# Kernel optimization log

Measured on AMD Instinct MI355X. Metric: run time of the kernel, lower is better.

Reference implementation:

```python
import jax, jax.numpy as jnp
import numpy as np

R = 16
LORA_ALPHA = 32
SCALING = LORA_ALPHA / R  # use_rslora=False -> alpha/r = 2.0


def fwht(x):
    """Normalized fast Walsh-Hadamard transform along last axis (power-of-2 dim)."""
    n = x.shape[-1]
    batch = x.shape[:-1]
    h = 1
    while h < n:  # static loop, log2(n) iterations
        x = x.reshape(*batch, n // (2 * h), 2, h)
        a = x[..., 0, :]
        b = x[..., 1, :]
        x = jnp.stack([a + b, a - b], axis=-2).reshape(*batch, n)
        h *= 2
    return x * np.float32(1.0 / np.sqrt(n))


def quant_int8_ste(x):
    """Simulated symmetric per-row int8 quantization with straight-through estimator."""
    s = jnp.max(jnp.abs(x), axis=-1, keepdims=True) * np.float32(1.0 / 127.0)
    s = jnp.maximum(s, np.float32(1e-8))
    q = jnp.clip(jnp.round(x / s), -127.0, 127.0) * s
    return x + jax.lax.stop_gradient(q - x)


def setup_inputs() -> dict:
    key = jax.random.key(0)
    k1, k2, k3, k4 = jax.random.split(key, 4)
    B, S, D_in, D_out = 4, 2048, 4096, 4096
    x = jax.random.normal(k1, (B, S, D_in), dtype=jnp.float32)
    weight = jax.random.normal(k2, (D_out, D_in), dtype=jnp.float32) * np.float32(0.02)
    lora_A = jax.random.normal(k3, (R, D_in), dtype=jnp.float32) * np.float32(0.02)
    lora_B = jax.random.normal(k4, (D_out, R), dtype=jnp.float32) * np.float32(0.02)
    return {"x": x, "weight": weight, "lora_A": lora_A, "lora_B": lora_B}


def reference(x, weight, lora_A, lora_B):
    B, S, D_in = x.shape
    x2 = x.reshape(-1, D_in)  # [B*S, D_in]
    # Hadamard-rotate + quantize both operands (rotation is orthogonal, so
    # (xH)(WH)^T == xW^T up to quantization error) then GEMM.
    xq = quant_int8_ste(fwht(x2))          # [B*S, D_in]
    wq = quant_int8_ste(fwht(weight))      # [D_out, D_in]
    out = xq @ wq.T                        # [B*S, D_out]
    # LoRA side path (dropout p=0): B(A x) * scaling
    lora = (x2 @ lora_A.T) @ lora_B.T * np.float32(SCALING)
    return (out + lora).reshape(B, S, -1)
```

## Files before the change

### kernel.cpp

```cpp
#include <hip/hip_runtime.h>
#include <stdint.h>

typedef int v4i __attribute__((ext_vector_type(4)));

#define GLD_LDS16(gp, lp)                                                              \
  __builtin_amdgcn_global_load_lds((const __attribute__((address_space(1))) void*)(gp), \
                                   (__attribute__((address_space(3))) void*)(lp), 16, 0, 0)

__device__ __forceinline__ v4i lds_read_b128(uint32_t off) {
  v4i r;
  asm volatile("ds_read_b128 %0, %1" : "=v"(r) : "v"(off));
  return r;
}

#define LGKM_FENCE()                                   \
  do {                                                 \
    asm volatile("s_waitcnt lgkmcnt(0)" ::: "memory"); \
    __builtin_amdgcn_sched_barrier(0);                 \
  } while (0)

__device__ __forceinline__ void fwht16(float v[16]) {
#pragma unroll
  for (int h = 1; h < 16; h <<= 1) {
#pragma unroll
    for (int i = 0; i < 16; ++i) {
      if (!(i & h)) {
        float a = v[i], b = v[i | h];
        v[i] = a + b;
        v[i | h] = a - b;
      }
    }
  }
}

__global__ __launch_bounds__(256) void fwht_quant_kernel(const float* __restrict__ X,
                                                         int8_t* __restrict__ Q,
                                                         float* __restrict__ S) {
  const int row = blockIdx.x;
  const int t = threadIdx.x;
  __shared__ float lds[4224];
  __shared__ float wred[4];

  const float* xr = X + (size_t)row * 4096;
  float v[16];
  {
    const float4* p = reinterpret_cast<const float4*>(xr) + t * 4;
    float4 a = p[0], b = p[1], c = p[2], d = p[3];
    v[0] = a.x; v[1] = a.y; v[2] = a.z; v[3] = a.w;
    v[4] = b.x; v[5] = b.y; v[6] = b.z; v[7] = b.w;
    v[8] = c.x; v[9] = c.y; v[10] = c.z; v[11] = c.w;
    v[12] = d.x; v[13] = d.y; v[14] = d.z; v[15] = d.w;
  }
  fwht16(v);
#pragma unroll
  for (int e = 0; e < 16; ++e) {
    int idx = t * 16 + e;
    lds[idx + (idx >> 5)] = v[e];
  }
  __syncthreads();
#pragma unroll
  for (int e = 0; e < 16; ++e) {
    int idx = ((t >> 4) << 8) + (e << 4) + (t & 15);
    v[e] = lds[idx + (idx >> 5)];
  }
  fwht16(v);
#pragma unroll
  for (int e = 0; e < 16; ++e) {
    int idx = ((t >> 4) << 8) + (e << 4) + (t & 15);
    lds[idx + (idx >> 5)] = v[e];
  }
  __syncthreads();
#pragma unroll
  for (int e = 0; e < 16; ++e) {
    int idx = (e << 8) + t;
    v[e] = lds[idx + (idx >> 5)];
  }
  fwht16(v);

  float m = 0.f;
#pragma unroll
  for (int e = 0; e < 16; ++e) {
    v[e] *= 0.015625f;
    m = fmaxf(m, fabsf(v[e]));
  }
#pragma unroll
  for (int off = 32; off > 0; off >>= 1) m = fmaxf(m, __shfl_xor(m, off));
  if ((t & 63) == 0) wred[t >> 6] = m;
  __syncthreads();
  m = fmaxf(fmaxf(wred[0], wred[1]), fmaxf(wred[2], wred[3]));
  const float s = fmaxf(m * (1.0f / 127.0f), 1e-8f);
  if (t == 0) S[row] = s;
  int8_t* qr = Q + (size_t)row * 4096;
#pragma unroll
  for (int e = 0; e < 16; ++e) {
    float q = rintf(v[e] / s);
    q = fminf(fmaxf(q, -127.f), 127.f);
    qr[(e << 8) + t] = (int8_t)(int)q;
  }
}

__global__ __launch_bounds__(256) void lora_t_partial_kernel(const float* __restrict__ X,
                                                             const float* __restrict__ A,
                                                             float* __restrict__ tpart) {
  __shared__ float As[16][512];
  const int t = threadIdx.x;
  const int kc = blockIdx.y;
  const int row = blockIdx.x * 256 + t;
  for (int i = t; i < 2048; i += 256) {
    int r = i >> 7;
    int c4 = i & 127;
    reinterpret_cast<float4*>(&As[r][0])[c4] =
        reinterpret_cast<const float4*>(A + (size_t)r * 4096 + kc * 512)[c4];
  }
  __syncthreads();
  float acc[16];
#pragma unroll
  for (int r = 0; r < 16; ++r) acc[r] = 0.f;
  const float* xr = X + (size_t)row * 4096 + kc * 512;
  for (int k = 0; k < 512; k += 4) {
    float4 xv = *reinterpret_cast<const float4*>(xr + k);
#pragma unroll
    for (int r = 0; r < 16; ++r) {
      float4 av = *reinterpret_cast<const float4*>(&As[r][k]);
      acc[r] += xv.x * av.x + xv.y * av.y + xv.z * av.z + xv.w * av.w;
    }
  }
  float* tp = tpart + ((size_t)kc * 8192 + row) * 16;
#pragma unroll
  for (int r = 0; r < 16; ++r) tp[r] = acc[r];
}

__global__ __launch_bounds__(256) void lora_t_reduce_kernel(const float* __restrict__ tpart,
                                                            float* __restrict__ tmat) {
  int i = blockIdx.x * 256 + threadIdx.x;
  float s = 0.f;
#pragma unroll
  for (int kc = 0; kc < 8; ++kc) s += tpart[(size_t)kc * 131072 + i];
  tmat[i] = s;
}

__global__ __launch_bounds__(512, 2) void gemm_i8_kernel(
    const int8_t* __restrict__ Aq, const int8_t* __restrict__ Bq,
    const float* __restrict__ Sx, const float* __restrict__ Sw,
    const float* __restrict__ Tm, const float* __restrict__ LB,
    float* __restrict__ out) {
  __shared__ __align__(16) char smem[131072];

  const int tid = threadIdx.x;
  const int lane = tid & 63;
  const int w = tid >> 6;
  const int wm = w >> 2;
  const int wn = w & 3;

  int bid = (int)blockIdx.x;
  bid = (bid & 7) * 64 + (bid >> 3);
  const int bm = bid >> 4;
  const int bn = bid & 15;

  const int8_t* Ag = Aq + (size_t)bm * 256 * 4096;
  const int8_t* Bg = Bq + (size_t)bn * 256 * 4096;

  const uint32_t sbase = (uint32_t)(uintptr_t)(void*)smem;

  const int L0 = w * 1024 + lane * 16;
  const int rS0 = L0 >> 6;
  const int rS1 = rS0 + 128;
  const int cS0 = (((lane & 3) ^ ((rS0 >> 1) & 3)) << 4);

#define STAGE(gbase, ldsOff, kByte)                                                      \
  do {                                                                                   \
    GLD_LDS16((gbase) + (size_t)rS0 * 4096 + (kByte) + cS0, smem + (ldsOff) + w * 1024); \
    GLD_LDS16((gbase) + (size_t)rS1 * 4096 + (kByte) + cS0,                              \
              smem + (ldsOff) + 8192 + w * 1024);                                        \
  } while (0)

  int aoff[8], boff[4];
  const int cc = lane >> 4;
#pragma unroll
  for (int mi = 0; mi < 8; ++mi) {
    int r = wm * 128 + mi * 16 + (lane & 15);
    aoff[mi] = r * 64 + ((cc ^ ((r >> 1) & 3)) << 4);
  }
#pragma unroll
  for (int ni = 0; ni < 4; ++ni) {
    int r = wn * 64 + ni * 16 + (lane & 15);
    boff[ni] = r * 64 + ((cc ^ ((r >> 1) & 3)) << 4);
  }

  v4i acc[8][4];
#pragma unroll
  for (int i = 0; i < 8; ++i)
#pragma unroll
    for (int n = 0; n < 4; ++n) {
      v4i z = {0, 0, 0, 0};
      acc[i][n] = z;
    }

  STAGE(Ag, 0, 0);
  STAGE(Bg, 32768, 0);
  STAGE(Ag, 16384, 64);
  STAGE(Bg, 49152, 64);
  asm volatile("s_waitcnt vmcnt(4)" ::: "memory");
  __builtin_amdgcn_s_barrier();
  __builtin_amdgcn_sched_barrier(0);

#define MFMA_CLUSTER(MH)                                                                  \
  do {                                                                                    \
    __builtin_amdgcn_s_setprio(1);                                                        \
    _Pragma("unroll") for (int i = 0; i < 4; ++i) _Pragma("unroll") for (int n = 0;       \
                                                                        n < 4; ++n)       \
        acc[(MH)*4 + i][n] =                                                              \
        __builtin_amdgcn_mfma_i32_16x16x64_i8(af[i], bf[n], acc[(MH)*4 + i][n], 0, 0, 0); \
    __builtin_amdgcn_s_setprio(0);                                                        \
  } while (0)

#pragma unroll 1
  for (int t = 0; t < 32; ++t) {
    const uint32_t Ab = sbase + (t & 1) * 65536;
    const uint32_t Bb = Ab + 32768;
    const int nx = ((t & 1) ^ 1) * 65536;
    const bool pf = (t + 1) < 32;
    const int kB = (t + 1) << 7;
    v4i af[4], bf[4];

    if (pf) STAGE(Ag, nx + 0, kB);
#pragma unroll
    for (int i = 0; i < 4; ++i) af[i] = lds_read_b128(Ab + aoff[i]);
#pragma unroll
    for (int n = 0; n < 4; ++n) bf[n] = lds_read_b128(Bb + boff[n]);
    __builtin_amdgcn_s_barrier();
    LGKM_FENCE();
    MFMA_CLUSTER(0);
    __builtin_amdgcn_s_barrier();

    if (pf) STAGE(Bg, nx + 32768, kB);
#pragma unroll
    for (int i = 0; i < 4; ++i) af[i] = lds_read_b128(Ab + aoff[4 + i]);
    __builtin_amdgcn_s_barrier();
    LGKM_FENCE();
    MFMA_CLUSTER(1);
    if (pf)
      asm volatile("s_waitcnt vmcnt(4)" ::: "memory");
    else
      asm volatile("s_waitcnt vmcnt(0)" ::: "memory");
    __builtin_amdgcn_s_barrier();
    __builtin_amdgcn_sched_barrier(0);

    if (pf) STAGE(Ag, nx + 16384, kB + 64);
#pragma unroll
    for (int i = 0; i < 4; ++i) af[i] = lds_read_b128(Ab + 16384 + aoff[i]);
#pragma unroll
    for (int n = 0; n < 4; ++n) bf[n] = lds_read_b128(Bb + 16384 + boff[n]);
    __builtin_amdgcn_s_barrier();
    LGKM_FENCE();
    MFMA_CLUSTER(0);
    __builtin_amdgcn_s_barrier();

    if (pf) STAGE(Bg, nx + 49152, kB + 64);
#pragma unroll
    for (int i = 0; i < 4; ++i) af[i] = lds_read_b128(Ab + 16384 + aoff[4 + i]);
    __builtin_amdgcn_s_barrier();
    LGKM_FENCE();
    MFMA_CLUSTER(1);
    if (pf) asm volatile("s_waitcnt vmcnt(4)" ::: "memory");
    __builtin_amdgcn_s_barrier();
    __builtin_amdgcn_sched_barrier(0);
  }

  __syncthreads();
  float* tl = (float*)smem;
  float* bl = (float*)(smem + 17408);
  for (int i = tid; i < 1024; i += 512) {
    int r = i >> 2, q4 = (i & 3) * 4;
    float4 tv = *reinterpret_cast<const float4*>(Tm + (size_t)(bm * 256 + r) * 16 + q4);
    tl[r * 17 + q4 + 0] = tv.x;
    tl[r * 17 + q4 + 1] = tv.y;
    tl[r * 17 + q4 + 2] = tv.z;
    tl[r * 17 + q4 + 3] = tv.w;
    float4 bv = *reinterpret_cast<const float4*>(LB + (size_t)(bn * 256 + r) * 16 + q4);
    bl[r * 17 + q4 + 0] = bv.x;
    bl[r * 17 + q4 + 1] = bv.y;
    bl[r * 17 + q4 + 2] = bv.z;
    bl[r * 17 + q4 + 3] = bv.w;
  }
  __syncthreads();

  float blv[4][16], swv[4];
#pragma unroll
  for (int ni = 0; ni < 4; ++ni) {
    int cl = wn * 64 + ni * 16 + (lane & 15);
    swv[ni] = Sw[bn * 256 + cl];
#pragma unroll
    for (int q = 0; q < 16; ++q) blv[ni][q] = bl[cl * 17 + q];
  }
#pragma unroll
  for (int mi = 0; mi < 8; ++mi) {
#pragma unroll
    for (int rr = 0; rr < 4; ++rr) {
      int rl = wm * 128 + mi * 16 + (lane >> 4) * 4 + rr;
      float sxv = Sx[bm * 256 + rl];
      float tv[16];
#pragma unroll
      for (int q = 0; q < 16; ++q) tv[q] = tl[rl * 17 + q];
      float* orow = out + (size_t)(bm * 256 + rl) * 4096 + bn * 256;
#pragma unroll
      for (int ni = 0; ni < 4; ++ni) {
        float dot = 0.f;
#pragma unroll
        for (int q = 0; q < 16; ++q) dot = fmaf(tv[q], blv[ni][q], dot);
        int cl = wn * 64 + ni * 16 + (lane & 15);
        orow[cl] = sxv * swv[ni] * (float)acc[mi][ni][rr] + 2.0f * dot;
      }
    }
  }
}

extern "C" void kernel_launch(void* const* d_in, const int* in_sizes, int n_in,
                              void* d_out, int out_size, void* d_ws, size_t ws_size,
                              hipStream_t stream) {
  const float* x = (const float*)d_in[0];
  const float* wgt = (const float*)d_in[1];
  const float* lA = (const float*)d_in[2];
  const float* lB = (const float*)d_in[3];
  float* out = (float*)d_out;

  char* ws = (char*)d_ws;
  int8_t* qx = (int8_t*)ws;
  int8_t* qw = (int8_t*)(ws + 33554432);
  float* sx = (float*)(ws + 50331648);
  float* sw = (float*)(ws + 50364416);
  float* tmat = (float*)(ws + 50380800);
  float* tpart = (float*)(ws + 50905088);

  fwht_quant_kernel<<<8192, 256, 0, stream>>>(x, qx, sx);
  fwht_quant_kernel<<<4096, 256, 0, stream>>>(wgt, qw, sw);
  lora_t_partial_kernel<<<dim3(32, 8), 256, 0, stream>>>(x, lA, tpart);
  lora_t_reduce_kernel<<<512, 256, 0, stream>>>(tpart, tmat);
  gemm_i8_kernel<<<512, 512, 0, stream>>>(qx, qw, sx, sw, tmat, lB, out);
}
```

Baseline: 273.8 us.

## Load full 128-byte K tile per stage with XOR swizzle and one barrier per iteration

Each pipeline stage now brings in a whole 128-byte K slice for A and B with four 16-byte global-to-LDS loads per thread. The rows are stored at a 128-byte pitch with an 8-way XOR swizzle, replacing the old two-half 64-byte layout. The main loop drops the many intra-iteration barriers and staged vmcnt waits in favour of a single wait and barrier at the end of each iteration. This cuts synchronisation overhead and lets the MFMA clusters run back to back. The cost is that prefetch overlap now depends on the whole iteration's compute hiding the full next-tile load, and there are more loads in flight per thread.

```diff
diff --git a/kernel.cpp b/kernel.cpp
--- a/kernel.cpp
+++ b/kernel.cpp
@@ -162,29 +162,27 @@
 
   const uint32_t sbase = (uint32_t)(uintptr_t)(void*)smem;
 
-  const int L0 = w * 1024 + lane * 16;
-  const int rS0 = L0 >> 6;
-  const int rS1 = rS0 + 128;
-  const int cS0 = (((lane & 3) ^ ((rS0 >> 1) & 3)) << 4);
-
-#define STAGE(gbase, ldsOff, kByte)                                                      \
-  do {                                                                                   \
-    GLD_LDS16((gbase) + (size_t)rS0 * 4096 + (kByte) + cS0, smem + (ldsOff) + w * 1024); \
-    GLD_LDS16((gbase) + (size_t)rS1 * 4096 + (kByte) + cS0,                              \
-              smem + (ldsOff) + 8192 + w * 1024);                                        \
+  const int row0 = w * 32 + (lane >> 3);
+  const int srcOff = (((lane & 7) ^ (lane >> 3)) << 4);
+
+#define STAGE_OP(gbase, ldsOpBase, tByte)                                        \
+  do {                                                                           \
+    _Pragma("unroll") for (int j = 0; j < 4; ++j)                                \
+        GLD_LDS16((gbase) + (size_t)(row0 + j * 8) * 4096 + (tByte) + srcOff,    \
+                  smem + (ldsOpBase) + w * 4096 + j * 1024);                     \
   } while (0)
 
   int aoff[8], boff[4];
-  const int cc = lane >> 4;
+  const int fch = (((lane >> 4) ^ (lane & 7)) << 4);
 #pragma unroll
   for (int mi = 0; mi < 8; ++mi) {
     int r = wm * 128 + mi * 16 + (lane & 15);
-    aoff[mi] = r * 64 + ((cc ^ ((r >> 1) & 3)) << 4);
+    aoff[mi] = r * 128 + fch;
   }
 #pragma unroll
   for (int ni = 0; ni < 4; ++ni) {
     int r = wn * 64 + ni * 16 + (lane & 15);
-    boff[ni] = r * 64 + ((cc ^ ((r >> 1) & 3)) << 4);
+    boff[ni] = 32768 + r * 128 + fch;
   }
 
   v4i acc[8][4];
@@ -196,15 +194,13 @@
       acc[i][n] = z;
     }
 
-  STAGE(Ag, 0, 0);
-  STAGE(Bg, 32768, 0);
-  STAGE(Ag, 16384, 64);
-  STAGE(Bg, 49152, 64);
-  asm volatile("s_waitcnt vmcnt(4)" ::: "memory");
+  STAGE_OP(Ag, 0, 0);
+  STAGE_OP(Bg, 32768, 0);
+  asm volatile("s_waitcnt vmcnt(0)" ::: "memory");
   __builtin_amdgcn_s_barrier();
   __builtin_amdgcn_sched_barrier(0);
 
-#define MFMA_CLUSTER(MH)                                                                  \
+#define MFMA16(MH)                                                                        \
   do {                                                                                    \
     __builtin_amdgcn_s_setprio(1);                                                        \
     _Pragma("unroll") for (int i = 0; i < 4; ++i) _Pragma("unroll") for (int n = 0;       \
@@ -217,52 +213,38 @@
 #pragma unroll 1
   for (int t = 0; t < 32; ++t) {
     const uint32_t Ab = sbase + (t & 1) * 65536;
-    const uint32_t Bb = Ab + 32768;
     const int nx = ((t & 1) ^ 1) * 65536;
     const bool pf = (t + 1) < 32;
-    const int kB = (t + 1) << 7;
+    const int tB = (t + 1) << 7;
     v4i af[4], bf[4];
 
-    if (pf) STAGE(Ag, nx + 0, kB);
+    if (pf) {
+      STAGE_OP(Ag, nx, tB);
+      STAGE_OP(Bg, nx + 32768, tB);
+    }
+
+#pragma unroll
+    for (int n = 0; n < 4; ++n) bf[n] = lds_read_b128(Ab + boff[n]);
 #pragma unroll
     for (int i = 0; i < 4; ++i) af[i] = lds_read_b128(Ab + aoff[i]);
-#pragma unroll
-    for (int n = 0; n < 4; ++n) bf[n] = lds_read_b128(Bb + boff[n]);
-    __builtin_amdgcn_s_barrier();
     LGKM_FENCE();
-    MFMA_CLUSTER(0);
-    __builtin_amdgcn_s_barrier();
-
-    if (pf) STAGE(Bg, nx + 32768, kB);
+    MFMA16(0);
 #pragma unroll
     for (int i = 0; i < 4; ++i) af[i] = lds_read_b128(Ab + aoff[4 + i]);
-    __builtin_amdgcn_s_barrier();
     LGKM_FENCE();
-    MFMA_CLUSTER(1);
-    if (pf)
-      asm volatile("s_waitcnt vmcnt(4)" ::: "memory");
-    else
-      asm volatile("s_waitcnt vmcnt(0)" ::: "memory");
-    __builtin_amdgcn_s_barrier();
-    __builtin_amdgcn_sched_barrier(0);
-
-    if (pf) STAGE(Ag, nx + 16384, kB + 64);
-#pragma unroll
-    for (int i = 0; i < 4; ++i) af[i] = lds_read_b128(Ab + 16384 + aoff[i]);
-#pragma unroll
-    for (int n = 0; n < 4; ++n) bf[n] = lds_read_b128(Bb + 16384 + boff[n]);
-    __builtin_amdgcn_s_barrier();
+    MFMA16(1);
+#pragma unroll
+    for (int n = 0; n < 4; ++n) bf[n] = lds_read_b128(Ab + (boff[n] ^ 64));
+#pragma unroll
+    for (int i = 0; i < 4; ++i) af[i] = lds_read_b128(Ab + (aoff[i] ^ 64));
     LGKM_FENCE();
-    MFMA_CLUSTER(0);
-    __builtin_amdgcn_s_barrier();
-
-    if (pf) STAGE(Bg, nx + 49152, kB + 64);
-#pragma unroll
-    for (int i = 0; i < 4; ++i) af[i] = lds_read_b128(Ab + 16384 + aoff[4 + i]);
-    __builtin_amdgcn_s_barrier();
+    MFMA16(0);
+#pragma unroll
+    for (int i = 0; i < 4; ++i) af[i] = lds_read_b128(Ab + (aoff[4 + i] ^ 64));
     LGKM_FENCE();
-    MFMA_CLUSTER(1);
-    if (pf) asm volatile("s_waitcnt vmcnt(4)" ::: "memory");
+    MFMA16(1);
+
+    asm volatile("s_waitcnt vmcnt(0)" ::: "memory");
     __builtin_amdgcn_s_barrier();
     __builtin_amdgcn_sched_barrier(0);
   }
```

Measured after the change: 265.8 us. 2.9% less time.
